# Optimization experiments

Hardware: AMD Instinct MI355X
Metric: run time of the kernel (lower is better)

Reference implementation:

```python
import jax, jax.numpy as jnp
import numpy as np

B, M, L, S = 8, 512, 31, 1  # batch, spatial, spectral bands, shots


def setup_inputs() -> dict:
    key = jax.random.key(0)
    k1, k2 = jax.random.split(key)
    x = jax.random.uniform(k1, (B, M, M, L, S), dtype=jnp.float32)
    H = jax.random.uniform(k2, (1, M, M, 1, S), dtype=jnp.float32)
    return {"x": x, "H": H}


def reference(x, H):
    # x: (B, M, M, L, S) spectral cube; H: (1, M, M, 1, S) coded aperture.
    # Original TF loop (pad + roll + slice + concat + reduce_sum) computes the
    # dispersed CASSI snapshot: Y[b,m,n,s] = sum_l (H*x)[b,m,n-l,l,s],
    # output width M + L - 1 (roll only wraps the zero padding for shifts < L).
    Bx, Mr, Mc, Lb, Sh = x.shape
    A = H * x  # (B, M, M, L, S) mask-modulated cube
    # Diagonal shift-accumulate via a single vectorized scatter-add.
    cols = (jnp.arange(Mc)[:, None] + jnp.arange(Lb)[None, :]).reshape(-1)  # (M*L,)
    Y = jnp.zeros((Bx, Mr, Mc + Lb - 1, Sh), dtype=x.dtype)
    Y = Y.at[:, :, cols, :].add(A.reshape(Bx, Mr, Mc * Lb, Sh))  # (B, M, M+L-1, S)
    Y = Y / jnp.max(Y)  # global max normalization as in the TF code
    return (Y, H)
```

## Files before the change

kernel.cpp:

```cpp
#include <hip/hip_runtime.h>


#define MDIM    512
#define LBANDS  31
#define WOUT    (MDIM + LBANDS - 1)
#define BATCH   8
#define ROWELEMS (MDIM * LBANDS)
#define CHUNK   256
#define NCHUNK  3
#define NBLK    (BATCH * MDIM * NCHUNK)
#define MAXLDSF 8872

__global__ __launch_bounds__(256, 4) void cassi_fwd_kernel(
    const float* __restrict__ x,
    const float* __restrict__ Hm,
    float* __restrict__ Y,
    float* __restrict__ bmaxs)
{
    __shared__ float xs[MAXLDSF];
    __shared__ float smax[4];

    const int tid = threadIdx.x;
    const int p   = blockIdx.x;
    const int lb    = ((p & 7) * (NBLK / 8)) + (p >> 3);
    const int bm    = lb / NCHUNK;
    const int chunk = lb - bm * NCHUNK;
    const int c0    = chunk * CHUNK;
    const int m     = bm & (MDIM - 1);

    int n0 = c0 - (LBANDS - 1); if (n0 < 0) n0 = 0;
    int n1 = c0 + CHUNK - 1;    if (n1 > MDIM - 1) n1 = MDIM - 1;
    const int gb   = (n0 * LBANDS) & ~3;
    const int nvec = ((n1 + 1) * LBANDS - gb + 3) >> 2;

    const float* __restrict__ xsl = x + (size_t)bm * ROWELEMS + gb;
    for (int v = tid; v < nvec; v += 256)
        __builtin_amdgcn_global_load_lds(
            (const __attribute__((address_space(1))) void*)(xsl + 4 * v),
            (__attribute__((address_space(3))) void*)(xs + 4 * v),
            16, 0, 0);
    __syncthreads();

    const int no = c0 + tid;
    const float* __restrict__ hrow = Hm + m * MDIM;
    const int bn = no - (LBANDS - 1);
    float acc = 0.0f;
    #pragma unroll
    for (int t = 0; t < LBANDS; ++t) {
        const int n  = bn + t;
        int nc = n;
        nc = nc < 0 ? 0 : nc;
        nc = nc > (MDIM - 1) ? (MDIM - 1) : nc;
        const float hv = (n == nc) ? hrow[nc] : 0.0f;
        const float xv = xs[nc * LBANDS + (LBANDS - 1 - t) - gb];
        acc = fmaf(hv, xv, acc);
    }
    float lmax = 0.0f;
    if (no < WOUT) {
        Y[(size_t)bm * WOUT + no] = acc;
        lmax = acc;
    }

    #pragma unroll
    for (int off = 32; off > 0; off >>= 1)
        lmax = fmaxf(lmax, __shfl_down(lmax, off, 64));
    if ((tid & 63) == 0) smax[tid >> 6] = lmax;
    __syncthreads();
    if (tid == 0)
        bmaxs[p] = fmaxf(fmaxf(smax[0], smax[1]), fmaxf(smax[2], smax[3]));
}

__global__ __launch_bounds__(1024) void cassi_norm_kernel(
    const float* __restrict__ Hm,
    float* __restrict__ out,
    const float* __restrict__ bmaxs,
    int ysize4, int total4)
{
    __shared__ float sred[16];
    float gm = 0.0f;
    const float4* __restrict__ w4 = (const float4*)bmaxs;
    for (int i = threadIdx.x; i < NBLK / 4; i += 1024) {
        const float4 v = w4[i];
        gm = fmaxf(fmaxf(gm, fmaxf(v.x, v.y)), fmaxf(v.z, v.w));
    }
    #pragma unroll
    for (int off = 32; off > 0; off >>= 1)
        gm = fmaxf(gm, __shfl_down(gm, off, 64));
    if ((threadIdx.x & 63) == 0) sred[threadIdx.x >> 6] = gm;
    __syncthreads();
    float bmax = sred[0];
    #pragma unroll
    for (int i = 1; i < 16; ++i) bmax = fmaxf(bmax, sred[i]);
    const float inv = 1.0f / bmax;

    const int idx = blockIdx.x * 1024 + threadIdx.x;
    if (idx < ysize4) {
        float4* __restrict__ o4 = (float4*)out;
        float4 v = o4[idx];
        v.x *= inv; v.y *= inv; v.z *= inv; v.w *= inv;
        o4[idx] = v;
    } else if (idx < total4) {
        const float4* __restrict__ h4 = (const float4*)Hm;
        ((float4*)out)[idx] = h4[idx - ysize4];
    }
}

extern "C" void kernel_launch(void* const* d_in, const int* in_sizes, int n_in,
                              void* d_out, int out_size, void* d_ws, size_t ws_size,
                              hipStream_t stream) {
    const float* x  = (const float*)d_in[0];
    const float* Hm = (const float*)d_in[1];
    float* out = (float*)d_out;
    float* ws  = (float*)d_ws;

    const int ysize4 = (BATCH * MDIM * WOUT) / 4;
    const int total4 = out_size / 4;

    cassi_fwd_kernel<<<NBLK, 256, 0, stream>>>(x, Hm, out, ws);
    cassi_norm_kernel<<<(total4 + 1023) / 1024, 1024, 0, stream>>>(
        Hm, out, ws, ysize4, total4);
}
```

Baseline: 56.78 us.

## Process full output row per block instead of three overlapping chunks

Each block now loads the whole 512x31 input row into LDS and computes all 542 outputs with 576 threads, replacing three 256-wide chunks per row that each reloaded an overlapping halo. This cuts the redundant global-to-LDS traffic and the block count. In exchange each block uses about 62 KB of LDS, which limits how many blocks fit per CU, and it drops the XCD-aware block swizzle.

```diff
diff --git a/kernel.cpp b/kernel.cpp
--- a/kernel.cpp
+++ b/kernel.cpp
@@ -6,57 +6,46 @@
 #define WOUT    (MDIM + LBANDS - 1)
 #define BATCH   8
 #define ROWELEMS (MDIM * LBANDS)
-#define CHUNK   256
-#define NCHUNK  3
-#define NBLK    (BATCH * MDIM * NCHUNK)
-#define MAXLDSF 8872
+#define NBLK    (BATCH * MDIM)
+#define TPB     576
 
-__global__ __launch_bounds__(256, 4) void cassi_fwd_kernel(
+__global__ __launch_bounds__(TPB) void cassi_fwd_kernel(
     const float* __restrict__ x,
     const float* __restrict__ Hm,
     float* __restrict__ Y,
     float* __restrict__ bmaxs)
 {
-    __shared__ float xs[MAXLDSF];
-    __shared__ float smax[4];
+    __shared__ float xs[ROWELEMS];
+    __shared__ float smax[9];
 
     const int tid = threadIdx.x;
-    const int p   = blockIdx.x;
-    const int lb    = ((p & 7) * (NBLK / 8)) + (p >> 3);
-    const int bm    = lb / NCHUNK;
-    const int chunk = lb - bm * NCHUNK;
-    const int c0    = chunk * CHUNK;
-    const int m     = bm & (MDIM - 1);
+    const int bm  = blockIdx.x;
+    const int m   = bm & (MDIM - 1);
 
-    int n0 = c0 - (LBANDS - 1); if (n0 < 0) n0 = 0;
-    int n1 = c0 + CHUNK - 1;    if (n1 > MDIM - 1) n1 = MDIM - 1;
-    const int gb   = (n0 * LBANDS) & ~3;
-    const int nvec = ((n1 + 1) * LBANDS - gb + 3) >> 2;
-
-    const float* __restrict__ xsl = x + (size_t)bm * ROWELEMS + gb;
-    for (int v = tid; v < nvec; v += 256)
+    const float* __restrict__ xrow = x + (size_t)bm * ROWELEMS;
+    for (int v = tid; v < ROWELEMS / 4; v += TPB)
         __builtin_amdgcn_global_load_lds(
-            (const __attribute__((address_space(1))) void*)(xsl + 4 * v),
+            (const __attribute__((address_space(1))) void*)(xrow + 4 * v),
             (__attribute__((address_space(3))) void*)(xs + 4 * v),
             16, 0, 0);
     __syncthreads();
 
-    const int no = c0 + tid;
-    const float* __restrict__ hrow = Hm + m * MDIM;
-    const int bn = no - (LBANDS - 1);
-    float acc = 0.0f;
-    #pragma unroll
-    for (int t = 0; t < LBANDS; ++t) {
-        const int n  = bn + t;
-        int nc = n;
-        nc = nc < 0 ? 0 : nc;
-        nc = nc > (MDIM - 1) ? (MDIM - 1) : nc;
-        const float hv = (n == nc) ? hrow[nc] : 0.0f;
-        const float xv = xs[nc * LBANDS + (LBANDS - 1 - t) - gb];
-        acc = fmaf(hv, xv, acc);
-    }
     float lmax = 0.0f;
-    if (no < WOUT) {
+    if (tid < WOUT) {
+        const int no = tid;
+        const float* __restrict__ hrow = Hm + m * MDIM;
+        const int bn = no - (LBANDS - 1);
+        float acc = 0.0f;
+        #pragma unroll
+        for (int t = 0; t < LBANDS; ++t) {
+            const int n  = bn + t;
+            int nc = n;
+            nc = nc < 0 ? 0 : nc;
+            nc = nc > (MDIM - 1) ? (MDIM - 1) : nc;
+            const float hv = (n == nc) ? hrow[nc] : 0.0f;
+            const float xv = xs[nc * LBANDS + (LBANDS - 1 - t)];
+            acc = fmaf(hv, xv, acc);
+        }
         Y[(size_t)bm * WOUT + no] = acc;
         lmax = acc;
     }
@@ -66,8 +55,12 @@
         lmax = fmaxf(lmax, __shfl_down(lmax, off, 64));
     if ((tid & 63) == 0) smax[tid >> 6] = lmax;
     __syncthreads();
-    if (tid == 0)
-        bmaxs[p] = fmaxf(fmaxf(smax[0], smax[1]), fmaxf(smax[2], smax[3]));
+    if (tid == 0) {
+        float bmax = smax[0];
+        #pragma unroll
+        for (int i = 1; i < 9; ++i) bmax = fmaxf(bmax, smax[i]);
+        bmaxs[bm] = bmax;
+    }
 }
 
 __global__ __launch_bounds__(1024) void cassi_norm_kernel(
@@ -116,7 +109,7 @@
     const int ysize4 = (BATCH * MDIM * WOUT) / 4;
     const int total4 = out_size / 4;
 
-    cassi_fwd_kernel<<<NBLK, 256, 0, stream>>>(x, Hm, out, ws);
+    cassi_fwd_kernel<<<NBLK, TPB, 0, stream>>>(x, Hm, out, ws);
     cassi_norm_kernel<<<(total4 + 1023) / 1024, 1024, 0, stream>>>(
         Hm, out, ws, ysize4, total4);
 }
```

After: 73.78 us. 1.3x slower.
